# Kernel tuning notes

Measured on AMD Instinct MI355X. Metric: run time of the kernel, lower is better.

## Reference

```python
import jax, jax.numpy as jnp
import numpy as np

MARGIN = 0.3
N, D = 8192, 1024
NUM_IDS = 751

def setup_inputs() -> dict:
    key = jax.random.key(0)
    k1, k2 = jax.random.split(key)
    inputs = jax.random.normal(k1, (N, D), dtype=jnp.float32)
    targets = jax.random.randint(k2, (N,), 0, NUM_IDS, dtype=jnp.int64)
    return {"inputs": inputs, "targets": targets}

def reference(inputs, targets):
    # sim[i,j] = <x_i, x_j>
    sim = jnp.matmul(inputs, inputs.T)  # [N, N]
    same = targets[:, None] == targets[None, :]  # [N, N] bool
    # positives: same label AND sim < 1 -> contribute (1 - sim)
    pos_mask = same & (sim < 1.0)
    pos_loss = jnp.sum(jnp.where(pos_mask, 1.0 - sim, 0.0), axis=1)  # [N]
    # negatives: different label AND sim > margin -> contribute sim
    neg_mask = (~same) & (sim > MARGIN)
    neg_loss = jnp.sum(jnp.where(neg_mask, sim, 0.0), axis=1)  # [N]
    n = inputs.shape[0]
    return jnp.sum(pos_loss + neg_loss) / n
```

## Files before the change

### kernel.cpp

```cpp
#include <hip/hip_runtime.h>
#include <stdint.h>

typedef float f32x4 __attribute__((ext_vector_type(4)));

#define NROWS 8192
#define DIM   1024
#define BK    128
#define NKT   (DIM / BK)
#define MARGIN 0.3f

#define GLOAD_LDS16(gp, lp)                                                    \
  __builtin_amdgcn_global_load_lds(                                            \
      (const __attribute__((address_space(1))) void*)(gp),                     \
      (__attribute__((address_space(3))) void*)(lp), 16, 0, 0)

__global__ __launch_bounds__(256) void cvt_f32_fp8(const float* __restrict__ in,
                                                   uint8_t* __restrict__ out,
                                                   float* __restrict__ loss) {
  if (blockIdx.x == 0 && threadIdx.x == 0) loss[0] = 0.0f;
  size_t i = ((size_t)blockIdx.x * 256 + threadIdx.x) * 16;
  float4 v0 = *(const float4*)(in + i);
  float4 v1 = *(const float4*)(in + i + 4);
  float4 v2 = *(const float4*)(in + i + 8);
  float4 v3 = *(const float4*)(in + i + 12);
  int w0 = 0, w1 = 0, w2 = 0, w3 = 0;
  w0 = __builtin_amdgcn_cvt_pk_fp8_f32(v0.x, v0.y, w0, false);
  w0 = __builtin_amdgcn_cvt_pk_fp8_f32(v0.z, v0.w, w0, true);
  w1 = __builtin_amdgcn_cvt_pk_fp8_f32(v1.x, v1.y, w1, false);
  w1 = __builtin_amdgcn_cvt_pk_fp8_f32(v1.z, v1.w, w1, true);
  w2 = __builtin_amdgcn_cvt_pk_fp8_f32(v2.x, v2.y, w2, false);
  w2 = __builtin_amdgcn_cvt_pk_fp8_f32(v2.z, v2.w, w2, true);
  w3 = __builtin_amdgcn_cvt_pk_fp8_f32(v3.x, v3.y, w3, false);
  w3 = __builtin_amdgcn_cvt_pk_fp8_f32(v3.z, v3.w, w3, true);
  uint4 p; p.x = (unsigned)w0; p.y = (unsigned)w1; p.z = (unsigned)w2; p.w = (unsigned)w3;
  *(uint4*)(out + i) = p;
}

__global__ __launch_bounds__(256, 3) void gram_loss(const uint8_t* __restrict__ A8,
                                                    const int* __restrict__ targets,
                                                    float* __restrict__ out) {
  __shared__ uint8_t As[128 * 128];
  __shared__ uint8_t Bs[128 * 128];
  __shared__ int tRow[128];
  __shared__ int tCol[128];
  __shared__ float wsum[4];

  int t = (blockIdx.x & 7) * 260 + (blockIdx.x >> 3);

  int bi = (int)(0.5f * (129.0f - __builtin_sqrtf(129.0f * 129.0f - 8.0f * (float)t)));
  if (bi < 0) bi = 0;
  if (bi > 63) bi = 63;
  while (bi < 63 && ((bi + 1) * (129 - (bi + 1))) / 2 <= t) ++bi;
  while (bi > 0 && (bi * (129 - bi)) / 2 > t) --bi;
  int bj = bi + (t - (bi * (129 - bi)) / 2);

  const int iBase = bi * 128;
  const int jBase = bj * 128;

  const int tid  = threadIdx.x;
  const int wave = tid >> 6;
  const int lane = tid & 63;

  if (tid < 128) tRow[tid] = targets[iBase + tid];
  else           tCol[tid - 128] = targets[jBase + tid - 128];

  const int lrow = lane >> 3;
  const int cg   = (lane & 7) ^ lrow;
  const uint8_t* gA = A8 + (size_t)(iBase + wave * 32 + lrow) * DIM + cg * 16;
  const uint8_t* gB = A8 + (size_t)(jBase + wave * 32 + lrow) * DIM + cg * 16;
  uint8_t* lA = &As[wave * 32 * 128];
  uint8_t* lB = &Bs[wave * 32 * 128];

  const int m0 = (wave >> 1) * 64;
  const int n0 = (wave & 1) * 64;
  const int fr = lane & 15;
  const int h  = lane >> 4;
  const int r7 = fr & 7;
  const int hHi = h >> 1;
  const int hLo = (h & 1) * 8;

  f32x4 acc[4][4] = {};

  for (int kt = 0; kt < NKT; ++kt) {
    __syncthreads();
    const int kOff = kt * BK;
#pragma unroll
    for (int l = 0; l < 4; ++l)
      GLOAD_LDS16(gA + (size_t)(l * 8) * DIM + kOff, lA + l * 8 * 128);
#pragma unroll
    for (int l = 0; l < 4; ++l)
      GLOAD_LDS16(gB + (size_t)(l * 8) * DIM + kOff, lB + l * 8 * 128);
    __syncthreads();

#pragma unroll
    for (int ks = 0; ks < 4; ++ks) {
      const int colOff = (((ks * 2 + hHi) ^ r7) * 16) + hLo;
      long af[4], bf[4];
#pragma unroll
      for (int mi = 0; mi < 4; ++mi)
        af[mi] = *(const long*)&As[(m0 + mi * 16 + fr) * 128 + colOff];
#pragma unroll
      for (int ni = 0; ni < 4; ++ni)
        bf[ni] = *(const long*)&Bs[(n0 + ni * 16 + fr) * 128 + colOff];
#pragma unroll
      for (int mi = 0; mi < 4; ++mi)
#pragma unroll
        for (int ni = 0; ni < 4; ++ni)
          acc[mi][ni] = __builtin_amdgcn_mfma_f32_16x16x32_fp8_fp8(
              af[mi], bf[ni], acc[mi][ni], 0, 0, 0);
    }
  }

  const int col = lane & 15;
  const int rquad = (lane >> 4) * 4;
  float lsum = 0.0f;
#pragma unroll
  for (int ni = 0; ni < 4; ++ni) {
    const int tj = tCol[n0 + ni * 16 + col];
#pragma unroll
    for (int mi = 0; mi < 4; ++mi) {
#pragma unroll
      for (int r = 0; r < 4; ++r) {
        float s = acc[mi][ni][r];
        int ti = tRow[m0 + mi * 16 + rquad + r];
        lsum += (ti == tj) ? (s < 1.0f ? 1.0f - s : 0.0f)
                           : (s > MARGIN ? s : 0.0f);
      }
    }
  }
  if (bi != bj) lsum *= 2.0f;

#pragma unroll
  for (int off = 32; off > 0; off >>= 1) lsum += __shfl_down(lsum, off, 64);
  if (lane == 0) wsum[wave] = lsum;
  __syncthreads();
  if (tid == 0)
    atomicAdd(out, (wsum[0] + wsum[1] + wsum[2] + wsum[3]) * (1.0f / (float)NROWS));
}

extern "C" void kernel_launch(void* const* d_in, const int* in_sizes, int n_in,
                              void* d_out, int out_size, void* d_ws, size_t ws_size,
                              hipStream_t stream) {
  const float* x = (const float*)d_in[0];
  const int* targets = (const int*)d_in[1];
  float* out = (float*)d_out;
  uint8_t* x8 = (uint8_t*)d_ws;

  cvt_f32_fp8<<<2048, 256, 0, stream>>>(x, x8, out);
  gram_loss<<<2080, 256, 0, stream>>>(x8, targets, out);
}
```

Measured before the change: 136.2 us.

## Double-buffer LDS tiles to overlap global loads with MFMA compute

Splits the A and B shared-memory tiles into two buffers and prefetches the next K tile with direct global-to-LDS loads while MFMAs run on the current one. Partial vmcnt waits and raw barriers replace the two __syncthreads per iteration, so load latency is hidden behind compute. LDS use doubles to 64KB per block, and launch bounds drop from 3 to 2 blocks per CU, which lowers occupancy.

```diff
diff --git a/kernel.cpp b/kernel.cpp
--- a/kernel.cpp
+++ b/kernel.cpp
@@ -36,11 +36,11 @@
   *(uint4*)(out + i) = p;
 }
 
-__global__ __launch_bounds__(256, 3) void gram_loss(const uint8_t* __restrict__ A8,
+__global__ __launch_bounds__(256, 2) void gram_loss(const uint8_t* __restrict__ A8,
                                                     const int* __restrict__ targets,
                                                     float* __restrict__ out) {
-  __shared__ uint8_t As[128 * 128];
-  __shared__ uint8_t Bs[128 * 128];
+  __shared__ uint8_t As[2][128 * 128];
+  __shared__ uint8_t Bs[2][128 * 128];
   __shared__ int tRow[128];
   __shared__ int tCol[128];
   __shared__ float wsum[4];
@@ -68,8 +68,7 @@
   const int cg   = (lane & 7) ^ lrow;
   const uint8_t* gA = A8 + (size_t)(iBase + wave * 32 + lrow) * DIM + cg * 16;
   const uint8_t* gB = A8 + (size_t)(jBase + wave * 32 + lrow) * DIM + cg * 16;
-  uint8_t* lA = &As[wave * 32 * 128];
-  uint8_t* lB = &Bs[wave * 32 * 128];
+  const int lOff = wave * 32 * 128;
 
   const int m0 = (wave >> 1) * 64;
   const int n0 = (wave & 1) * 64;
@@ -81,35 +80,54 @@
 
   f32x4 acc[4][4] = {};
 
-  for (int kt = 0; kt < NKT; ++kt) {
-    __syncthreads();
-    const int kOff = kt * BK;
-#pragma unroll
-    for (int l = 0; l < 4; ++l)
-      GLOAD_LDS16(gA + (size_t)(l * 8) * DIM + kOff, lA + l * 8 * 128);
-#pragma unroll
-    for (int l = 0; l < 4; ++l)
-      GLOAD_LDS16(gB + (size_t)(l * 8) * DIM + kOff, lB + l * 8 * 128);
-    __syncthreads();
+#define STAGE(b_, kt_)                                                         \
+  { const int kO_ = (kt_) * BK;                                                \
+    _Pragma("unroll")                                                          \
+    for (int l = 0; l < 4; ++l)                                                \
+      GLOAD_LDS16(gA + (size_t)(l * 8) * DIM + kO_, &As[b_][lOff + l * 8 * 128]); \
+    _Pragma("unroll")                                                          \
+    for (int l = 0; l < 4; ++l)                                                \
+      GLOAD_LDS16(gB + (size_t)(l * 8) * DIM + kO_, &Bs[b_][lOff + l * 8 * 128]); }
 
-#pragma unroll
-    for (int ks = 0; ks < 4; ++ks) {
-      const int colOff = (((ks * 2 + hHi) ^ r7) * 16) + hLo;
-      long af[4], bf[4];
-#pragma unroll
-      for (int mi = 0; mi < 4; ++mi)
-        af[mi] = *(const long*)&As[(m0 + mi * 16 + fr) * 128 + colOff];
-#pragma unroll
-      for (int ni = 0; ni < 4; ++ni)
-        bf[ni] = *(const long*)&Bs[(n0 + ni * 16 + fr) * 128 + colOff];
-#pragma unroll
-      for (int mi = 0; mi < 4; ++mi)
-#pragma unroll
-        for (int ni = 0; ni < 4; ++ni)
-          acc[mi][ni] = __builtin_amdgcn_mfma_f32_16x16x32_fp8_fp8(
-              af[mi], bf[ni], acc[mi][ni], 0, 0, 0);
-    }
+#define COMPUTE(b_)                                                            \
+  _Pragma("unroll")                                                            \
+  for (int ks = 0; ks < 4; ++ks) {                                             \
+    const int colOff = (((ks * 2 + hHi) ^ r7) * 16) + hLo;                     \
+    long af[4], bf[4];                                                         \
+    _Pragma("unroll")                                                          \
+    for (int mi = 0; mi < 4; ++mi)                                             \
+      af[mi] = *(const long*)&As[b_][(m0 + mi * 16 + fr) * 128 + colOff];      \
+    _Pragma("unroll")                                                          \
+    for (int ni = 0; ni < 4; ++ni)                                             \
+      bf[ni] = *(const long*)&Bs[b_][(n0 + ni * 16 + fr) * 128 + colOff];      \
+    _Pragma("unroll")                                                          \
+    for (int mi = 0; mi < 4; ++mi)                                             \
+      _Pragma("unroll")                                                        \
+      for (int ni = 0; ni < 4; ++ni)                                           \
+        acc[mi][ni] = __builtin_amdgcn_mfma_f32_16x16x32_fp8_fp8(              \
+            af[mi], bf[ni], acc[mi][ni], 0, 0, 0);                             \
   }
+
+  STAGE(0, 0);
+
+#pragma unroll 2
+  for (int kt = 0; kt < NKT - 1; ++kt) {
+    const int cur = kt & 1;
+    STAGE(cur ^ 1, kt + 1);
+    asm volatile("s_waitcnt vmcnt(8)" ::: "memory");
+    __builtin_amdgcn_s_barrier();
+    asm volatile("" ::: "memory");
+    COMPUTE(cur);
+    asm volatile("" ::: "memory");
+    __builtin_amdgcn_s_barrier();
+  }
+  asm volatile("s_waitcnt vmcnt(0)" ::: "memory");
+  __builtin_amdgcn_s_barrier();
+  asm volatile("" ::: "memory");
+  COMPUTE((NKT - 1) & 1);
+
+#undef STAGE
+#undef COMPUTE
 
   const int col = lane & 15;
   const int rquad = (lane >> 4) * 4;
```

New measurement: 151.8 us. +11.4%, slower.

## Overlap next K-tile global-to-LDS load with MFMA compute via register prefetch

Applied to the files above, without the earlier changes.

Each iteration now reads the whole K-tile's A/B fragments from LDS into registers, then hits a barrier and issues the global_load_lds for the next tile into the same buffers. The 64 MFMAs run while that load is in flight, which is meant to hide global memory latency without a second LDS buffer. The cost is more VGPRs for the fragment arrays (32 longs per thread), which may reduce occupancy under launch_bounds(256,3). Sched barriers keep the compiler from interleaving the loads and MFMAs.

```diff
diff --git a/kernel.cpp b/kernel.cpp
--- a/kernel.cpp
+++ b/kernel.cpp
@@ -81,35 +81,48 @@
 
   f32x4 acc[4][4] = {};
 
+#define STAGE(kt_)                                                             \
+  { const int kO_ = (kt_) * BK;                                                \
+    _Pragma("unroll")                                                          \
+    for (int l = 0; l < 4; ++l)                                                \
+      GLOAD_LDS16(gA + (size_t)(l * 8) * DIM + kO_, lA + l * 8 * 128);         \
+    _Pragma("unroll")                                                          \
+    for (int l = 0; l < 4; ++l)                                                \
+      GLOAD_LDS16(gB + (size_t)(l * 8) * DIM + kO_, lB + l * 8 * 128); }
+
+  STAGE(0);
+  asm volatile("s_waitcnt vmcnt(0)" ::: "memory");
+  __builtin_amdgcn_s_barrier();
+
   for (int kt = 0; kt < NKT; ++kt) {
-    __syncthreads();
-    const int kOff = kt * BK;
-#pragma unroll
-    for (int l = 0; l < 4; ++l)
-      GLOAD_LDS16(gA + (size_t)(l * 8) * DIM + kOff, lA + l * 8 * 128);
-#pragma unroll
-    for (int l = 0; l < 4; ++l)
-      GLOAD_LDS16(gB + (size_t)(l * 8) * DIM + kOff, lB + l * 8 * 128);
-    __syncthreads();
-
+    long af[4][4], bf[4][4];
 #pragma unroll
     for (int ks = 0; ks < 4; ++ks) {
       const int colOff = (((ks * 2 + hHi) ^ r7) * 16) + hLo;
-      long af[4], bf[4];
 #pragma unroll
       for (int mi = 0; mi < 4; ++mi)
-        af[mi] = *(const long*)&As[(m0 + mi * 16 + fr) * 128 + colOff];
+        af[ks][mi] = *(const long*)&As[(m0 + mi * 16 + fr) * 128 + colOff];
 #pragma unroll
       for (int ni = 0; ni < 4; ++ni)
-        bf[ni] = *(const long*)&Bs[(n0 + ni * 16 + fr) * 128 + colOff];
+        bf[ks][ni] = *(const long*)&Bs[(n0 + ni * 16 + fr) * 128 + colOff];
+    }
+    asm volatile("s_waitcnt lgkmcnt(0)" ::: "memory");
+    __builtin_amdgcn_s_barrier();
+    if (kt + 1 < NKT) STAGE(kt + 1);
+    __builtin_amdgcn_sched_barrier(0);
+#pragma unroll
+    for (int ks = 0; ks < 4; ++ks)
 #pragma unroll
       for (int mi = 0; mi < 4; ++mi)
 #pragma unroll
         for (int ni = 0; ni < 4; ++ni)
           acc[mi][ni] = __builtin_amdgcn_mfma_f32_16x16x32_fp8_fp8(
-              af[mi], bf[ni], acc[mi][ni], 0, 0, 0);
-    }
+              af[ks][mi], bf[ks][ni], acc[mi][ni], 0, 0, 0);
+    __builtin_amdgcn_sched_barrier(0);
+    asm volatile("s_waitcnt vmcnt(0)" ::: "memory");
+    __builtin_amdgcn_s_barrier();
   }
+#undef STAGE
 
   const int col = lane & 15;
   const int rquad = (lane >> 4) * 4;
```

New measurement: 137.7 us. No clear change (+1.1%).
